# Kernel tuning notes

Measured on AMD Instinct MI355X. Metric: run time of the kernel, lower is better.

Reference implementation:

```python
import jax, jax.numpy as jnp
import numpy as np

N = 100000
E = 1600000
D_IN = 128
D_OUT = 128
BN_EPS = 1e-5


def setup_inputs() -> dict:
    key = jax.random.key(0)
    k_x, k_src, k_dst, k_val, k_w = jax.random.split(key, 5)
    x = jax.random.normal(k_x, (N, D_IN), dtype=jnp.float32)
    edge_src = jax.random.randint(k_src, (E,), 0, N, dtype=jnp.int64)
    edge_dst = jax.random.randint(k_dst, (E,), 0, N, dtype=jnp.int64)
    edge_vals = jax.random.uniform(k_val, (E,), dtype=jnp.float32)
    # kaiming-uniform-like init for weight
    bound = float(np.sqrt(6.0 / D_IN))
    weight = jax.random.uniform(k_w, (D_IN, D_OUT), dtype=jnp.float32,
                                minval=-bound, maxval=bound)
    bias = jnp.zeros((D_OUT,), dtype=jnp.float32)
    gamma = jnp.ones((D_OUT,), dtype=jnp.float32)   # BatchNorm weight
    beta = jnp.zeros((D_OUT,), dtype=jnp.float32)   # BatchNorm bias
    return {"x": x, "edge_src": edge_src, "edge_dst": edge_dst,
            "edge_vals": edge_vals, "weight": weight, "bias": bias,
            "gamma": gamma, "beta": beta}


def reference(x, edge_src, edge_dst, edge_vals, weight, bias, gamma, beta):
    # SpMM: out[dst] += val * x[src]  (adj @ x with adj in COO form)
    msgs = x[edge_src] * edge_vals[:, None]            # [E, D_IN]
    agg = jax.ops.segment_sum(msgs, edge_dst, num_segments=N)  # [N, D_IN]
    # Dense linear
    h = jnp.dot(agg, weight) + bias                     # [N, D_OUT]
    # BatchNorm1d (training mode: batch statistics, biased variance)
    mean = jnp.mean(h, axis=0)
    var = jnp.mean(jnp.square(h - mean), axis=0)
    h_norm = (h - mean) * jax.lax.rsqrt(var + BN_EPS)
    return h_norm * gamma + beta
```

## Files before the change

### kernel.cpp

```cpp
#include <hip/hip_runtime.h>
#include <math.h>

#define D 128
#define BSHIFT 9
#define BROWS 512
#define TILE 8192
constexpr float BN_EPS = 1e-5f;
typedef unsigned long long ull;

__device__ __forceinline__ unsigned f2bf_rne(float f) {
    unsigned u = __float_as_uint(f);
    return (u + 0x7FFFu + ((u >> 16) & 1u)) >> 16;
}
__device__ __forceinline__ float bf_lo(unsigned u) { return __uint_as_float(u << 16); }
__device__ __forceinline__ float bf_hi(unsigned u) { return __uint_as_float(u & 0xFFFF0000u); }

__global__ __launch_bounds__(256) void phase1_kernel(
    const float* __restrict__ A,
    const float* __restrict__ W,
    unsigned* __restrict__ yb,
    int n,
    const int* __restrict__ esrc, const int* __restrict__ edst,
    const float* __restrict__ evals,
    uint2* __restrict__ slices,
    int* __restrict__ ofs_t,
    int B, int nwgA, int E)
{
    __shared__ __align__(16) char smem[81920];
    const int tid = threadIdx.x;

    if ((int)blockIdx.x < nwgA) {
        int* h   = (int*)smem;
        int* ps  = h + 256;
        int* cur = ps + 256;
        const int wg = blockIdx.x;
        const int e0 = wg * TILE;
        const int e1 = min(e0 + TILE, E);

        h[tid] = 0;
        __syncthreads();
        for (int e = e0 + tid; e < e1; e += 256)
            atomicAdd(&h[edst[e] >> BSHIFT], 1);
        __syncthreads();

        const int v = h[tid];
        ps[tid] = v;
        __syncthreads();
        for (int off = 1; off < 256; off <<= 1) {
            int t = (tid >= off) ? ps[tid - off] : 0;
            __syncthreads();
            if (tid >= off) ps[tid] += t;
            __syncthreads();
        }
        const int excl = ps[tid] - v;
        if (tid < B) {
            cur[tid] = excl;
            ofs_t[(size_t)tid * nwgA + wg] = excl;
        }
        if (tid == 0) ofs_t[(size_t)B * nwgA + wg] = e1 - e0;
        __syncthreads();

        uint2* slice = slices + (size_t)wg * TILE;
        for (int e = e0 + tid; e < e1; e += 256) {
            int d = edst[e];
            int b = d >> BSHIFT;
            int p = atomicAdd(&cur[b], 1);
            uint2 rec;
            rec.x = (unsigned)(d & (BROWS - 1)) | ((unsigned)esrc[e] << BSHIFT);
            rec.y = __float_as_uint(evals[e]);
            slice[p] = rec;
        }
    } else {
        float* sW = (float*)smem;
        float (*sA)[128] = (float(*)[128])(smem + 65536);

        const float4* W4  = (const float4*)W;
        float4*       sW4 = (float4*)sW;
#pragma unroll
        for (int i = 0; i < 16; i++) sW4[tid + 256 * i] = W4[tid + 256 * i];

        const int row0 = (blockIdx.x - nwgA) * 32;
        const float4* A4  = (const float4*)(A + (size_t)row0 * D);
        float4*       sA4 = (float4*)&sA[0][0];
#pragma unroll
        for (int i = 0; i < 4; i++) {
            int idx = tid + 256 * i;
            sA4[idx] = ((size_t)row0 * D + (size_t)idx * 4 < (size_t)n * D)
                           ? A4[idx] : make_float4(0.f, 0.f, 0.f, 0.f);
        }
        __syncthreads();

        const int tx = tid & 31;
        const int ty = tid >> 5;
        const int c0 = tx * 4;

        float acc[4][4] = {};
        for (int k0 = 0; k0 < 128; k0 += 4) {
            float4 a[4];
#pragma unroll
            for (int j = 0; j < 4; j++)
                a[j] = *(const float4*)&sA[ty + 8 * j][k0];
#pragma unroll
            for (int kk = 0; kk < 4; kk++) {
                const float4 w = *(const float4*)&sW[(k0 + kk) * 128 + c0];
                const float ak[4] = { kk == 0 ? a[0].x : kk == 1 ? a[0].y : kk == 2 ? a[0].z : a[0].w,
                                      kk == 0 ? a[1].x : kk == 1 ? a[1].y : kk == 2 ? a[1].z : a[1].w,
                                      kk == 0 ? a[2].x : kk == 1 ? a[2].y : kk == 2 ? a[2].z : a[2].w,
                                      kk == 0 ? a[3].x : kk == 1 ? a[3].y : kk == 2 ? a[3].z : a[3].w };
#pragma unroll
                for (int j = 0; j < 4; j++) {
                    acc[j][0] += ak[j] * w.x;
                    acc[j][1] += ak[j] * w.y;
                    acc[j][2] += ak[j] * w.z;
                    acc[j][3] += ak[j] * w.w;
                }
            }
        }

#pragma unroll
        for (int j = 0; j < 4; j++) {
            const int row = row0 + ty + 8 * j;
            if (row < n) {
                uint2 o;
                o.x = f2bf_rne(acc[j][0]) | (f2bf_rne(acc[j][1]) << 16);
                o.y = f2bf_rne(acc[j][2]) | (f2bf_rne(acc[j][3]) << 16);
                ((uint2*)(yb + (size_t)row * 64))[tx] = o;
            }
        }
    }
}

__global__ __launch_bounds__(1024) void binB_kernel(
    const uint2* __restrict__ slices,
    const int* __restrict__ ofs_t,
    int* __restrict__ rowptr,
    ull* __restrict__ csr,
    int B, int nwgA, int n)
{
    __shared__ int srow[256];
    __shared__ int erow[256];
    __shared__ int red[256];
    __shared__ int hist[BROWS];
    __shared__ int curs[BROWS];
    __shared__ int ps[BROWS];
    __shared__ int s_bbase;

    const int tid  = threadIdx.x;
    const int b    = blockIdx.x;
    const int w    = tid >> 6;
    const int lane = tid & 63;

    for (int i = tid; i < nwgA; i += 1024) {
        srow[i] = ofs_t[(size_t)b * nwgA + i];
        erow[i] = ofs_t[(size_t)(b + 1) * nwgA + i];
    }
    if (tid < BROWS) hist[tid] = 0;
    __syncthreads();

    if (tid < 256) red[tid] = (tid < nwgA) ? srow[tid] : 0;
    __syncthreads();
    for (int off = 128; off > 0; off >>= 1) {
        if (tid < off) red[tid] += red[tid + off];
        __syncthreads();
    }
    if (tid == 0) s_bbase = red[0];
    __syncthreads();

    for (int wg = w; wg < nwgA; wg += 16) {
        const int s = srow[wg];
        const int e = erow[wg];
        const uint2* run = slices + (size_t)wg * TILE;
        for (int i = s + lane; i < e; i += 64)
            atomicAdd(&hist[run[i].x & (BROWS - 1)], 1);
    }
    __syncthreads();

    int v0 = 0;
    if (tid < BROWS) { v0 = hist[tid]; ps[tid] = v0; }
    __syncthreads();
    for (int off = 1; off < BROWS; off <<= 1) {
        int t = 0;
        if (tid < BROWS && tid >= off) t = ps[tid - off];
        __syncthreads();
        if (tid < BROWS) ps[tid] += t;
        __syncthreads();
    }
    if (tid < BROWS) {
        const int excl = s_bbase + ps[tid] - v0;
        curs[tid] = excl;
        const int r = (b << BSHIFT) + tid;
        if (r < n) rowptr[r] = excl + v0;
    }
    __syncthreads();

    for (int wg = w; wg < nwgA; wg += 16) {
        const int s = srow[wg];
        const int e = erow[wg];
        const uint2* run = slices + (size_t)wg * TILE;
        for (int i = s + lane; i < e; i += 64) {
            uint2 r = run[i];
            int pos = atomicAdd(&curs[r.x & (BROWS - 1)], 1);
            csr[pos] = ((ull)r.y << 32) | (r.x >> BSHIFT);
        }
    }
}

__global__ __launch_bounds__(256) void spmm_stats_kernel(
    const unsigned* __restrict__ yb,
    const int* __restrict__ rowptr,
    const ull* __restrict__ csr,
    float* __restrict__ h,
    float* __restrict__ stats,
    int n)
{
    __shared__ float ssum[128];
    __shared__ float ssq[128];
    const int tid  = threadIdx.x;
    const int wv   = tid >> 6;
    const int lane = tid & 63;
    const int rbase = blockIdx.x * 64 + wv * 16;

    if (tid < 128) { ssum[tid] = 0.f; ssq[tid] = 0.f; }
    __syncthreads();

    float sx = 0.f, sy = 0.f, qx = 0.f, qy = 0.f;
    for (int i = 0; i < 16; i++) {
        const int r = rbase + i;
        if (r >= n) break;
        const int start = r ? rowptr[r - 1] : 0;
        const int end   = rowptr[r];

        float ax = 0.f, ay = 0.f;
        int e = start;
        for (; e + 7 < end; e += 8) {
            ull e0 = csr[e],     e1 = csr[e + 1], e2 = csr[e + 2], e3 = csr[e + 3];
            ull e4 = csr[e + 4], e5 = csr[e + 5], e6 = csr[e + 6], e7 = csr[e + 7];
            unsigned u0 = yb[(size_t)(unsigned)e0 * 64 + lane];
            unsigned u1 = yb[(size_t)(unsigned)e1 * 64 + lane];
            unsigned u2 = yb[(size_t)(unsigned)e2 * 64 + lane];
            unsigned u3 = yb[(size_t)(unsigned)e3 * 64 + lane];
            unsigned u4 = yb[(size_t)(unsigned)e4 * 64 + lane];
            unsigned u5 = yb[(size_t)(unsigned)e5 * 64 + lane];
            unsigned u6 = yb[(size_t)(unsigned)e6 * 64 + lane];
            unsigned u7 = yb[(size_t)(unsigned)e7 * 64 + lane];
            float v0 = __uint_as_float((unsigned)(e0 >> 32));
            float v1 = __uint_as_float((unsigned)(e1 >> 32));
            float v2 = __uint_as_float((unsigned)(e2 >> 32));
            float v3 = __uint_as_float((unsigned)(e3 >> 32));
            float v4 = __uint_as_float((unsigned)(e4 >> 32));
            float v5 = __uint_as_float((unsigned)(e5 >> 32));
            float v6 = __uint_as_float((unsigned)(e6 >> 32));
            float v7 = __uint_as_float((unsigned)(e7 >> 32));
            ax += v0 * bf_lo(u0) + v1 * bf_lo(u1) + v2 * bf_lo(u2) + v3 * bf_lo(u3)
                + v4 * bf_lo(u4) + v5 * bf_lo(u5) + v6 * bf_lo(u6) + v7 * bf_lo(u7);
            ay += v0 * bf_hi(u0) + v1 * bf_hi(u1) + v2 * bf_hi(u2) + v3 * bf_hi(u3)
                + v4 * bf_hi(u4) + v5 * bf_hi(u5) + v6 * bf_hi(u6) + v7 * bf_hi(u7);
        }
        for (; e + 3 < end; e += 4) {
            ull e0 = csr[e], e1 = csr[e + 1], e2 = csr[e + 2], e3 = csr[e + 3];
            unsigned u0 = yb[(size_t)(unsigned)e0 * 64 + lane];
            unsigned u1 = yb[(size_t)(unsigned)e1 * 64 + lane];
            unsigned u2 = yb[(size_t)(unsigned)e2 * 64 + lane];
            unsigned u3 = yb[(size_t)(unsigned)e3 * 64 + lane];
            float v0 = __uint_as_float((unsigned)(e0 >> 32));
            float v1 = __uint_as_float((unsigned)(e1 >> 32));
            float v2 = __uint_as_float((unsigned)(e2 >> 32));
            float v3 = __uint_as_float((unsigned)(e3 >> 32));
            ax += v0 * bf_lo(u0) + v1 * bf_lo(u1) + v2 * bf_lo(u2) + v3 * bf_lo(u3);
            ay += v0 * bf_hi(u0) + v1 * bf_hi(u1) + v2 * bf_hi(u2) + v3 * bf_hi(u3);
        }
        for (; e < end; e++) {
            ull ed = csr[e];
            unsigned u = yb[(size_t)(unsigned)ed * 64 + lane];
            float v = __uint_as_float((unsigned)(ed >> 32));
            ax += v * bf_lo(u);
            ay += v * bf_hi(u);
        }
        ((float2*)(h + (size_t)r * D))[lane] = make_float2(ax, ay);
        sx += ax; sy += ay; qx += ax * ax; qy += ay * ay;
    }

    atomicAdd(&ssum[2 * lane],     sx);
    atomicAdd(&ssum[2 * lane + 1], sy);
    atomicAdd(&ssq[2 * lane],      qx);
    atomicAdd(&ssq[2 * lane + 1],  qy);
    __syncthreads();
    if (tid < 128) {
        atomicAdd(&stats[tid],       ssum[tid]);
        atomicAdd(&stats[128 + tid], ssq[tid]);
    }
}

__global__ __launch_bounds__(256) void bn_apply_kernel(
    float* __restrict__ h,
    const float* __restrict__ stats,
    const float* __restrict__ gamma,
    const float* __restrict__ beta,
    int n)
{
    __shared__ float s_scale[128];
    __shared__ float s_shift[128];
    const int tid = threadIdx.x;
    if (tid < 128) {
        const float invn = 1.0f / (float)n;
        const float mean = stats[tid] * invn;
        const float var  = stats[128 + tid] * invn - mean * mean;
        const float inv  = rsqrtf(var + BN_EPS);
        const float g    = gamma[tid] * inv;
        s_scale[tid] = g;
        s_shift[tid] = beta[tid] - mean * g;
    }
    __syncthreads();

    float4* h4 = (float4*)h;
    const size_t total = (size_t)n * D / 4;
    const size_t stride = (size_t)gridDim.x * blockDim.x;
    for (size_t i = (size_t)blockIdx.x * blockDim.x + tid; i < total; i += stride) {
        float4 v = h4[i];
        const int c = (int)((i * 4) & (D - 1));
        v.x = v.x * s_scale[c]     + s_shift[c];
        v.y = v.y * s_scale[c + 1] + s_shift[c + 1];
        v.z = v.z * s_scale[c + 2] + s_shift[c + 2];
        v.w = v.w * s_scale[c + 3] + s_shift[c + 3];
        h4[i] = v;
    }
}

__global__ __launch_bounds__(256) void spmm_atomic_kernel(
    const float* __restrict__ x,
    const int* __restrict__ esrc, const int* __restrict__ edst,
    const float* __restrict__ eval, float* __restrict__ agg, int E)
{
    int wave  = (blockIdx.x * blockDim.x + threadIdx.x) >> 6;
    int lane  = threadIdx.x & 63;
    int nwave = (gridDim.x * blockDim.x) >> 6;
    for (int e = wave; e < E; e += nwave) {
        int   s = esrc[e];
        int   d = edst[e];
        float v = eval[e];
        const float2 xv = ((const float2*)(x + (size_t)s * D))[lane];
        float* ar = agg + (size_t)d * D + lane * 2;
        atomicAdd(ar,     xv.x * v);
        atomicAdd(ar + 1, xv.y * v);
    }
}

__global__ __launch_bounds__(256) void gemm_stats_kernel(
    const float* __restrict__ A,
    const float* __restrict__ W,
    float* __restrict__ h,
    float* __restrict__ stats,
    int n)
{
    __shared__ float sW[128 * 128];
    __shared__ float sA[32][128];
    const int tid = threadIdx.x;
    const float4* W4  = (const float4*)W;
    float4*       sW4 = (float4*)sW;
#pragma unroll
    for (int i = 0; i < 16; i++) sW4[tid + 256 * i] = W4[tid + 256 * i];
    const int row0 = blockIdx.x * 32;
    const float4* A4  = (const float4*)(A + (size_t)row0 * D);
    float4*       sA4 = (float4*)&sA[0][0];
#pragma unroll
    for (int i = 0; i < 4; i++) {
        int idx = tid + 256 * i;
        sA4[idx] = ((size_t)row0 * D + (size_t)idx * 4 < (size_t)n * D)
                       ? A4[idx] : make_float4(0.f, 0.f, 0.f, 0.f);
    }
    __syncthreads();
    const int tx = tid & 31, ty = tid >> 5, c0 = tx * 4;
    float acc[4][4] = {};
    for (int k = 0; k < 128; k++) {
        const float4 w = *(const float4*)&sW[k * 128 + c0];
#pragma unroll
        for (int j = 0; j < 4; j++) {
            const float a = sA[ty + 8 * j][k];
            acc[j][0] += a * w.x; acc[j][1] += a * w.y;
            acc[j][2] += a * w.z; acc[j][3] += a * w.w;
        }
    }
#pragma unroll
    for (int j = 0; j < 4; j++) {
        const int row = row0 + ty + 8 * j;
        if (row < n)
            *(float4*)&h[(size_t)row * D + c0] =
                make_float4(acc[j][0], acc[j][1], acc[j][2], acc[j][3]);
    }
    __syncthreads();
    float* csum = &sA[0][0];
    float* csq  = csum + 128;
    if (tid < 128) { csum[tid] = 0.f; csq[tid] = 0.f; }
    __syncthreads();
#pragma unroll
    for (int c = 0; c < 4; c++) {
        float s = 0.f, q = 0.f;
#pragma unroll
        for (int j = 0; j < 4; j++) { s += acc[j][c]; q += acc[j][c] * acc[j][c]; }
        atomicAdd(&csum[c0 + c], s);
        atomicAdd(&csq[c0 + c], q);
    }
    __syncthreads();
    if (tid < 128) {
        atomicAdd(&stats[tid],       csum[tid]);
        atomicAdd(&stats[128 + tid], csq[tid]);
    }
}

extern "C" void kernel_launch(void* const* d_in, const int* in_sizes, int n_in,
                              void* d_out, int out_size, void* d_ws, size_t ws_size,
                              hipStream_t stream)
{
    const float* x     = (const float*)d_in[0];
    const int*   esrc  = (const int*)d_in[1];
    const int*   edst  = (const int*)d_in[2];
    const float* evals = (const float*)d_in[3];
    const float* W     = (const float*)d_in[4];
    const float* gamma = (const float*)d_in[6];
    const float* beta  = (const float*)d_in[7];
    float* out = (float*)d_out;

    const int n = in_sizes[0] / D;
    const int E = in_sizes[1];

    const int B     = (n + BROWS - 1) >> BSHIFT;
    const int nwgA  = (E + TILE - 1) / TILE;
    const int ngemm = (n + 31) / 32;

    unsigned* yb     = (unsigned*)d_ws;
    float*    stats  = (float*)(yb + (size_t)n * 64);
    int*      ofs_t  = (int*)(stats + 256);
    int*      rowptr = ofs_t + (size_t)(B + 1) * nwgA;
    size_t    w_off  = (size_t)n * 64 + 256 + (size_t)(B + 1) * nwgA + n;
    w_off += (w_off & 1);
    uint2*    slices = (uint2*)((unsigned*)d_ws + w_off);
    ull*      csr    = (ull*)(slices + (size_t)nwgA * TILE);
    const size_t need = (w_off + (size_t)nwgA * TILE * 2 + (size_t)E * 2) * 4;

    if (ws_size >= need && B <= 256 && nwgA <= 256) {
        hipMemsetAsync(stats, 0, 256 * 4, stream);
        phase1_kernel<<<nwgA + ngemm, 256, 0, stream>>>(
            x, W, yb, n, esrc, edst, evals, slices, ofs_t, B, nwgA, E);
        binB_kernel<<<B, 1024, 0, stream>>>(
            slices, ofs_t, rowptr, csr, B, nwgA, n);
        spmm_stats_kernel<<<(n + 63) / 64, 256, 0, stream>>>(
            yb, rowptr, csr, out, stats, n);
        bn_apply_kernel<<<2048, 256, 0, stream>>>(out, stats, gamma, beta, n);
    } else {
        float* agg = (float*)d_ws;
        float* st  = agg + (size_t)n * D;
        hipMemsetAsync(d_ws, 0, ((size_t)n * D + 256) * 4, stream);
        spmm_atomic_kernel<<<4096, 256, 0, stream>>>(x, esrc, edst, evals, agg, E);
        gemm_stats_kernel<<<(n + 31) / 32, 256, 0, stream>>>(agg, W, out, st, n);
        bn_apply_kernel<<<2048, 256, 0, stream>>>(out, st, gamma, beta, n);
    }
}
```

Measured before the change: 311.7 us.

## Restructure SpMM gather into half-wave edge pairs with software-pipelined chunks

The SpMM-stats kernel now splits each wavefront into two 32-lane halves that process alternating edges. Each lane gathers 8 bytes (4 bf16 features) instead of 4, and the two halves are combined with a shuffle when a row is flushed. Rows are streamed as one continuous edge sequence across the wave's 16 rows, with row pointers cached in shared memory. Chunks of 8 edges are double-buffered so index loads for the next chunk overlap the FMAs of the current one. The aim is better load width and memory-level parallelism across short rows, at the cost of more control flow, lambda-inlined branching, and extra registers.

```diff
diff --git a/kernel.cpp b/kernel.cpp
--- a/kernel.cpp
+++ b/kernel.cpp
@@ -213,77 +213,130 @@
     float* __restrict__ stats,
     int n)
 {
+    __shared__ int   rp[65];
     __shared__ float ssum[128];
     __shared__ float ssq[128];
-    const int tid  = threadIdx.x;
-    const int wv   = tid >> 6;
-    const int lane = tid & 63;
-    const int rbase = blockIdx.x * 64 + wv * 16;
+
+    const int tid       = threadIdx.x;
+    const int blockRow0 = blockIdx.x * 64;
 
     if (tid < 128) { ssum[tid] = 0.f; ssq[tid] = 0.f; }
-    __syncthreads();
-
-    float sx = 0.f, sy = 0.f, qx = 0.f, qy = 0.f;
-    for (int i = 0; i < 16; i++) {
-        const int r = rbase + i;
-        if (r >= n) break;
-        const int start = r ? rowptr[r - 1] : 0;
-        const int end   = rowptr[r];
-
-        float ax = 0.f, ay = 0.f;
-        int e = start;
-        for (; e + 7 < end; e += 8) {
-            ull e0 = csr[e],     e1 = csr[e + 1], e2 = csr[e + 2], e3 = csr[e + 3];
-            ull e4 = csr[e + 4], e5 = csr[e + 5], e6 = csr[e + 6], e7 = csr[e + 7];
-            unsigned u0 = yb[(size_t)(unsigned)e0 * 64 + lane];
-            unsigned u1 = yb[(size_t)(unsigned)e1 * 64 + lane];
-            unsigned u2 = yb[(size_t)(unsigned)e2 * 64 + lane];
-            unsigned u3 = yb[(size_t)(unsigned)e3 * 64 + lane];
-            unsigned u4 = yb[(size_t)(unsigned)e4 * 64 + lane];
-            unsigned u5 = yb[(size_t)(unsigned)e5 * 64 + lane];
-            unsigned u6 = yb[(size_t)(unsigned)e6 * 64 + lane];
-            unsigned u7 = yb[(size_t)(unsigned)e7 * 64 + lane];
-            float v0 = __uint_as_float((unsigned)(e0 >> 32));
-            float v1 = __uint_as_float((unsigned)(e1 >> 32));
-            float v2 = __uint_as_float((unsigned)(e2 >> 32));
-            float v3 = __uint_as_float((unsigned)(e3 >> 32));
-            float v4 = __uint_as_float((unsigned)(e4 >> 32));
-            float v5 = __uint_as_float((unsigned)(e5 >> 32));
-            float v6 = __uint_as_float((unsigned)(e6 >> 32));
-            float v7 = __uint_as_float((unsigned)(e7 >> 32));
-            ax += v0 * bf_lo(u0) + v1 * bf_lo(u1) + v2 * bf_lo(u2) + v3 * bf_lo(u3)
-                + v4 * bf_lo(u4) + v5 * bf_lo(u5) + v6 * bf_lo(u6) + v7 * bf_lo(u7);
-            ay += v0 * bf_hi(u0) + v1 * bf_hi(u1) + v2 * bf_hi(u2) + v3 * bf_hi(u3)
-                + v4 * bf_hi(u4) + v5 * bf_hi(u5) + v6 * bf_hi(u6) + v7 * bf_hi(u7);
-        }
-        for (; e + 3 < end; e += 4) {
-            ull e0 = csr[e], e1 = csr[e + 1], e2 = csr[e + 2], e3 = csr[e + 3];
-            unsigned u0 = yb[(size_t)(unsigned)e0 * 64 + lane];
-            unsigned u1 = yb[(size_t)(unsigned)e1 * 64 + lane];
-            unsigned u2 = yb[(size_t)(unsigned)e2 * 64 + lane];
-            unsigned u3 = yb[(size_t)(unsigned)e3 * 64 + lane];
-            float v0 = __uint_as_float((unsigned)(e0 >> 32));
-            float v1 = __uint_as_float((unsigned)(e1 >> 32));
-            float v2 = __uint_as_float((unsigned)(e2 >> 32));
-            float v3 = __uint_as_float((unsigned)(e3 >> 32));
-            ax += v0 * bf_lo(u0) + v1 * bf_lo(u1) + v2 * bf_lo(u2) + v3 * bf_lo(u3);
-            ay += v0 * bf_hi(u0) + v1 * bf_hi(u1) + v2 * bf_hi(u2) + v3 * bf_hi(u3);
-        }
-        for (; e < end; e++) {
-            ull ed = csr[e];
-            unsigned u = yb[(size_t)(unsigned)ed * 64 + lane];
-            float v = __uint_as_float((unsigned)(ed >> 32));
-            ax += v * bf_lo(u);
-            ay += v * bf_hi(u);
-        }
-        ((float2*)(h + (size_t)r * D))[lane] = make_float2(ax, ay);
-        sx += ax; sy += ay; qx += ax * ax; qy += ay * ay;
-    }
-
-    atomicAdd(&ssum[2 * lane],     sx);
-    atomicAdd(&ssum[2 * lane + 1], sy);
-    atomicAdd(&ssq[2 * lane],      qx);
-    atomicAdd(&ssq[2 * lane + 1],  qy);
+    if (tid < 65) {
+        int idx = blockRow0 + tid - 1;
+        rp[tid] = (idx < 0) ? 0 : rowptr[min(idx, n - 1)];
+    }
+    __syncthreads();
+
+    const int wv    = tid >> 6;
+    const int lane  = tid & 63;
+    const int half  = lane >> 5;
+    const int li    = lane & 31;
+    const int rbase = blockRow0 + wv * 16;
+
+    float s0 = 0.f, s1 = 0.f, s2 = 0.f, s3 = 0.f;
+    float q0 = 0.f, q1 = 0.f, q2 = 0.f, q3 = 0.f;
+
+    if (rbase < n) {
+        const int r1 = min(rbase + 16, n);
+
+        int curRow  = rbase;
+        int eNext   = rp[curRow - blockRow0];
+        int eRowEnd = rp[curRow - blockRow0 + 1];
+        int accRow  = rbase;
+        float a0 = 0.f, a1 = 0.f, a2 = 0.f, a3 = 0.f;
+
+        auto flushTo = [&](int newRow) {
+            float t0 = a0 + __shfl_down(a0, 32);
+            float t1 = a1 + __shfl_down(a1, 32);
+            float t2 = a2 + __shfl_down(a2, 32);
+            float t3 = a3 + __shfl_down(a3, 32);
+            if (lane < 32) {
+                *(float4*)&h[(size_t)accRow * D + li * 4] =
+                    make_float4(t0, t1, t2, t3);
+                s0 += t0; s1 += t1; s2 += t2; s3 += t3;
+                q0 += t0 * t0; q1 += t1 * t1; q2 += t2 * t2; q3 += t3 * t3;
+            }
+            a0 = a1 = a2 = a3 = 0.f;
+            for (int z = accRow + 1; z < newRow; ++z)
+                if (lane < 32)
+                    *(float4*)&h[(size_t)z * D + li * 4] =
+                        make_float4(0.f, 0.f, 0.f, 0.f);
+            accRow = newRow;
+        };
+
+        auto build = [&](ull (&c)[8], unsigned& ridPack, unsigned& vmask) -> int {
+            int cnt = 0; ridPack = 0u; vmask = 0u;
+            bool done = false;
+#pragma unroll
+            for (int j = 0; j < 8; ++j) {
+                if (!done) {
+                    while (eNext >= eRowEnd) {
+                        if (curRow + 1 >= r1) { done = true; break; }
+                        ++curRow;
+                        eNext   = rp[curRow - blockRow0];
+                        eRowEnd = rp[curRow - blockRow0 + 1];
+                    }
+                    if (!done) {
+                        ridPack |= (unsigned)(curRow - rbase) << (4 * j);
+                        int  ei    = eNext + half;
+                        bool valid = ei < eRowEnd;
+                        int  ci    = valid ? ei : (eRowEnd - 1);
+                        c[j] = csr[ci];
+                        vmask |= (valid ? 1u : 0u) << j;
+                        eNext += 2;
+                        ++cnt;
+                    }
+                }
+            }
+            return cnt;
+        };
+
+        uint2 u[8];
+        auto gather = [&](const ull (&c)[8], int cnt) {
+#pragma unroll
+            for (int j = 0; j < 8; ++j)
+                if (j < cnt)
+                    u[j] = *(const uint2*)(yb + (size_t)(unsigned)c[j] * 64 + 2 * li);
+        };
+        auto fmaChunk = [&](const ull (&c)[8], unsigned ridPack, unsigned vmask,
+                            int cnt) {
+#pragma unroll
+            for (int j = 0; j < 8; ++j) {
+                if (j < cnt) {
+                    int r = rbase + (int)((ridPack >> (4 * j)) & 15u);
+                    if (r != accRow) flushTo(r);
+                    float v = ((vmask >> j) & 1u)
+                                  ? __uint_as_float((unsigned)(c[j] >> 32))
+                                  : 0.f;
+                    a0 += v * bf_lo(u[j].x);
+                    a1 += v * bf_hi(u[j].x);
+                    a2 += v * bf_lo(u[j].y);
+                    a3 += v * bf_hi(u[j].y);
+                }
+            }
+        };
+
+        ull cA[8], cB[8];
+        unsigned ridA, vmA, ridB, vmB;
+        int cntA = build(cA, ridA, vmA);
+        while (cntA > 0) {
+            gather(cA, cntA);
+            int cntB = build(cB, ridB, vmB);
+            fmaChunk(cA, ridA, vmA, cntA);
+            if (cntB == 0) break;
+            gather(cB, cntB);
+            cntA = build(cA, ridA, vmA);
+            fmaChunk(cB, ridB, vmB, cntB);
+        }
+        flushTo(r1);
+    }
+
+    if (rbase < n && lane < 32) {
+        atomicAdd(&ssum[4 * li + 0], s0); atomicAdd(&ssum[4 * li + 1], s1);
+        atomicAdd(&ssum[4 * li + 2], s2); atomicAdd(&ssum[4 * li + 3], s3);
+        atomicAdd(&ssq [4 * li + 0], q0); atomicAdd(&ssq [4 * li + 1], q1);
+        atomicAdd(&ssq [4 * li + 2], q2); atomicAdd(&ssq [4 * li + 3], q3);
+    }
     __syncthreads();
     if (tid < 128) {
         atomicAdd(&stats[tid],       ssum[tid]);
```

New measurement: 311.3 us. Within noise of the previous version (-0.1%).
